# Kernel optimization log

Measured on AMD Instinct MI355X. Metric: run time of the kernel, lower is better.

The kernel has to match this reference:

```python
import jax, jax.numpy as jnp
import numpy as np

B, S, H, E, K, DFF = 4, 2048, 1024, 8, 2, 4096


def setup_inputs() -> dict:
    key = jax.random.key(0)
    k0, k1, k2, k3 = jax.random.split(key, 4)
    sc = 0.02
    return {
        "x": jax.random.normal(k0, (B, S, H), jnp.float32),
        "gate_W": jax.random.normal(k1, (H, E), jnp.float32) * sc,
        "gate_b": jnp.zeros((E,), jnp.float32),
        "W1": jax.random.normal(k2, (H, DFF), jnp.float32) * sc,
        "b1": jnp.zeros((DFF,), jnp.float32),
        "W2": jax.random.normal(k3, (DFF, H), jnp.float32) * sc,
        "b2": jnp.zeros((H,), jnp.float32),
    }


def reference(x, gate_W, gate_b, W1, b1, W2, b2):
    b, s, h = x.shape
    x_flat = x.reshape(-1, h)                      # [T, H]
    gate_scores = x_flat @ gate_W + gate_b         # [T, E]
    top_k_scores, top_k_idx = jax.lax.top_k(gate_scores, K)   # [T, K]
    top_k_w = jax.nn.softmax(top_k_scores, axis=-1)           # [T, K]

    # All experts share the same weights (ModuleList reuses one module), so
    # sum_i w_i * expert_i(x) == expert(x) * sum_i w_i. top_k indices are
    # unique per token, so the per-token combine weight is sum of top-k weights.
    hdd = jax.nn.gelu(x_flat @ W1 + b1, approximate=False)    # [T, DFF]
    y = hdd @ W2 + b2                                         # [T, H]
    tok_w = top_k_w.sum(axis=-1)                              # [T] (== 1.0)
    output = (y * tok_w[:, None]).reshape(b, s, h)

    expert_load = gate_scores.mean(axis=0)                    # [E]
    aux_loss = (expert_load ** 2).sum()
    exp_counts = jnp.zeros((E,), jnp.int32).at[top_k_idx.ravel()].add(1)
    return output, aux_loss, exp_counts
```

## Files before the change

### kernel.cpp

```cpp
#include <hip/hip_runtime.h>
#include <hip/hip_bf16.h>
#include <math.h>

#define Tn   8192
#define Hn   1024
#define En   8
#define DFFn 4096

typedef __attribute__((ext_vector_type(8))) short bf16x8;
typedef __attribute__((ext_vector_type(8))) unsigned short u16x8;
typedef __attribute__((ext_vector_type(4))) float f32x4;

static __device__ inline unsigned short f2bf(float f) {
    __hip_bfloat16 h = __float2bfloat16(f);
    return __builtin_bit_cast(unsigned short, h);
}

__global__ __launch_bounds__(256) void prep(
    const float* __restrict__ W1, unsigned short* __restrict__ W1t,
    const float* __restrict__ W2, unsigned short* __restrict__ W2t,
    const float* __restrict__ x, const float* __restrict__ gW,
    const float* __restrict__ gb, unsigned short* __restrict__ xbf,
    float* __restrict__ tokw, float* __restrict__ load_sum,
    int* __restrict__ counts)
{
    __shared__ float smem[8 * 1024 + En];
    __shared__ int   s_cnt[En];
    const int tid = threadIdx.x;
    const int id  = blockIdx.x;

    if (id < 512) {
        const float* src; unsigned short* dst; int SR, SC, tb;
        if (id < 256) { src = W1; dst = W1t; SR = Hn;   SC = DFFn; tb = id; }
        else          { src = W2; dst = W2t; SR = DFFn; SC = Hn;   tb = id - 256; }
        const int tcs = SC >> 7;
        const int tr  = tb / tcs, tc = tb - tr * tcs;
        const int r0  = tr << 7, c0 = tc << 7;
        unsigned short* tile = (unsigned short*)smem;

        #pragma unroll
        for (int i = 0; i < 16; ++i) {
            int idx = tid + i * 256;
            int r = idx >> 5, c4 = (idx & 31) << 2;
            float4 v = *(const float4*)(src + (size_t)(r0 + r) * SC + c0 + c4);
            int cs = c4 ^ (((r >> 3) & 7) << 2);
            ushort4 pk;
            pk.x = f2bf(v.x); pk.y = f2bf(v.y);
            pk.z = f2bf(v.z); pk.w = f2bf(v.w);
            *(ushort4*)(tile + r * 128 + cs) = pk;
        }
        __syncthreads();
        #pragma unroll
        for (int i = 0; i < 8; ++i) {
            int idx = tid + i * 256;
            int n = idx >> 4, kg = idx & 15, k0 = kg << 3;
            int s = (kg & 7) << 2;
            u16x8 o;
            #pragma unroll
            for (int j = 0; j < 8; ++j)
                o[j] = tile[(k0 + j) * 128 + (n ^ s)];
            *(u16x8*)(dst + (size_t)(c0 + n) * SR + r0 + k0) = o;
        }
        return;
    }

    const int gid = id - 512;
    float* gwt    = smem;
    float* s_load = smem + 8 * 1024;
    if (tid < En) { s_load[tid] = 0.f; s_cnt[tid] = 0; }
    #pragma unroll
    for (int i = 0; i < 32; ++i) {
        int f = tid + i * 256;
        gwt[(f & 7) * 1024 + (f >> 3)] = gW[f];
    }
    __syncthreads();

    const int lane = tid & 63;
    const int wv   = tid >> 6;

    for (int tok = gid * 4 + wv; tok < Tn; tok += 4096) {
        const float4* xr = (const float4*)(x + (size_t)tok * Hn);
        float acc[8] = {0.f,0.f,0.f,0.f,0.f,0.f,0.f,0.f};
        #pragma unroll
        for (int j = 0; j < Hn / 256; ++j) {
            int h4 = j * 64 + lane;
            float4 xv = xr[h4];
            ushort4 pk;
            pk.x = f2bf(xv.x); pk.y = f2bf(xv.y);
            pk.z = f2bf(xv.z); pk.w = f2bf(xv.w);
            ((ushort4*)xbf)[(size_t)tok * (Hn / 4) + h4] = pk;
            #pragma unroll
            for (int e = 0; e < 8; ++e) {
                const float4 w = *(const float4*)(gwt + e * 1024 + h4 * 4);
                acc[e] += xv.x * w.x + xv.y * w.y + xv.z * w.z + xv.w * w.w;
            }
        }
        #pragma unroll
        for (int e = 0; e < 8; ++e) {
            float v = acc[e];
            #pragma unroll
            for (int off = 32; off > 0; off >>= 1) v += __shfl_xor(v, off, 64);
            acc[e] = v + gb[e];
        }
        if (lane == 0) {
            #pragma unroll
            for (int e = 0; e < 8; ++e) atomicAdd(&s_load[e], acc[e]);
            int i1 = 0; float v1 = acc[0];
            #pragma unroll
            for (int e = 1; e < 8; ++e) if (acc[e] > v1) { v1 = acc[e]; i1 = e; }
            int i2 = -1; float v2 = -3.0e38f;
            #pragma unroll
            for (int e = 0; e < 8; ++e) if (e != i1 && acc[e] > v2) { v2 = acc[e]; i2 = e; }
            atomicAdd(&s_cnt[i1], 1);
            atomicAdd(&s_cnt[i2], 1);
            float e2 = __expf(v2 - v1);
            float t  = 1.0f + e2;
            tokw[tok] = 1.0f / t + e2 / t;
        }
    }
    __syncthreads();
    if (tid < En) {
        atomicAdd(&load_sum[tid], s_load[tid]);
        atomicAdd(&counts[tid],   s_cnt[tid]);
    }
}

static __device__ inline bf16x8 ldsfrag(const char* base, int row, int chunk) {
    return *(const bf16x8*)(base + row * 128 + (((chunk) ^ (row & 7)) << 4));
}

template<int BN, int WM, int WN, int EPI>
__global__ __launch_bounds__(512, 2) void gemm8(
    const __hip_bfloat16* __restrict__ A,
    const __hip_bfloat16* __restrict__ Bt,
    const float* __restrict__ bias,
    const float* __restrict__ tokw,
    void* __restrict__ C, int N, int K, int nx,
    const float* __restrict__ load_sum, const int* __restrict__ counts,
    float* __restrict__ out_tail, int nblk)
{
    constexpr int BM = 256;
    constexpr int MR = (BM / WM) / 16;
    constexpr int NR = (BN / WN) / 16;
    constexpr int AU = BM / 64;
    constexpr int BU = BN / 64;
    constexpr int ABYTES = BM * 64 * 2;
    constexpr int BBYTES = BN * 64 * 2;
    constexpr int TILEB  = ABYTES + BBYTES;

    extern __shared__ char lds[];

    const int tid = threadIdx.x;
    const int id  = blockIdx.x;

    if (EPI == 0 && id >= nblk) {
        if (tid == 0) {
            float aux = 0.f;
            #pragma unroll
            for (int e = 0; e < En; ++e) {
                float m = load_sum[e] * (1.0f / (float)Tn);
                aux += m * m;
            }
            out_tail[0] = aux;
            #pragma unroll
            for (int e = 0; e < En; ++e) out_tail[1 + e] = (float)counts[e];
        }
        return;
    }

    int wg = id;
    { int xcd = wg & 7, idx = wg >> 3; wg = xcd * (nblk >> 3) + idx; }
    const int by = wg / nx, bx = wg % nx;
    const int m0 = by * BM, n0 = bx * BN;

    const int lane = tid & 63;
    const int wid  = tid >> 6;
    const int wn   = wid % WN;
    const int wm   = wid / WN;
    const int wrow = wm * (BM / WM);
    const int wcol = wn * (BN / WN);
    const int fr   = lane & 15;
    const int fq   = lane >> 4;

    const int sr = tid >> 3;
    const int sc = (tid & 7) ^ (sr & 7);
    unsigned aOff[AU], bOff[BU];
    #pragma unroll
    for (int u = 0; u < AU; ++u)
        aOff[u] = (unsigned)((m0 + u * 64 + sr) * K + sc * 8);
    #pragma unroll
    for (int u = 0; u < BU; ++u)
        bOff[u] = (unsigned)((n0 + u * 64 + sr) * K + sc * 8);

#define STA(b, u, kt) __builtin_amdgcn_global_load_lds( \
    (const __attribute__((address_space(1))) void*)(A + aOff[u] + (unsigned)(kt) * 64u), \
    (__attribute__((address_space(3))) void*)(lds + (b) * TILEB + (u) * 8192 + tid * 16), 16, 0, 0)
#define STB(b, u, kt) __builtin_amdgcn_global_load_lds( \
    (const __attribute__((address_space(1))) void*)(Bt + bOff[u] + (unsigned)(kt) * 64u), \
    (__attribute__((address_space(3))) void*)(lds + (b) * TILEB + ABYTES + (u) * 8192 + tid * 16), 16, 0, 0)

    bf16x8 af[MR / 2][2];
    bf16x8 bfr[4][2];
    f32x4  acc[MR][NR];
    const f32x4 zero = {0.f, 0.f, 0.f, 0.f};
    #pragma unroll
    for (int i = 0; i < MR; ++i)
        #pragma unroll
        for (int j = 0; j < NR; ++j) acc[i][j] = zero;

#define RD_A1(b, half, m_) do { _Pragma("unroll") \
    for (int ks_ = 0; ks_ < 2; ++ks_) \
        af[m_][ks_] = ldsfrag(lds + (b) * TILEB, \
            wrow + ((half) * (MR / 2) + (m_)) * 16 + fr, ks_ * 4 + fq); } while (0)
#define RD_B1(b, nn) do { _Pragma("unroll") \
    for (int ks_ = 0; ks_ < 2; ++ks_) \
        bfr[nn][ks_] = ldsfrag(lds + (b) * TILEB + ABYTES, \
            wcol + (nn) * 16 + fr, ks_ * 4 + fq); } while (0)

#define MFMA_M(hm, hn, m_) do { _Pragma("unroll") \
    for (int n_ = 0; n_ < 2; ++n_) { _Pragma("unroll") \
        for (int ks_ = 0; ks_ < 2; ++ks_) \
            acc[(hm) * (MR / 2) + (m_)][(hn) * 2 + n_] = \
                __builtin_amdgcn_mfma_f32_16x16x32_bf16( \
                    af[m_][ks_], bfr[(hn) * 2 + n_][ks_], \
                    acc[(hm) * (MR / 2) + (m_)][(hn) * 2 + n_], 0, 0, 0); } } while (0)
#define MFMA_N(hm, nn) do { _Pragma("unroll") \
    for (int m_ = 0; m_ < MR / 2; ++m_) { _Pragma("unroll") \
        for (int ks_ = 0; ks_ < 2; ++ks_) \
            acc[(hm) * (MR / 2) + m_][nn] = \
                __builtin_amdgcn_mfma_f32_16x16x32_bf16( \
                    af[m_][ks_], bfr[nn][ks_], \
                    acc[(hm) * (MR / 2) + m_][nn], 0, 0, 0); } } while (0)

#define MFMA1_N(hm, nn) do { _Pragma("unroll") \
    for (int m_ = 0; m_ < MR / 2; ++m_) { _Pragma("unroll") \
        for (int ks_ = 0; ks_ < 2; ++ks_) \
            acc[(hm) * (MR / 2) + m_][nn] = \
                __builtin_amdgcn_mfma_f32_16x16x32_bf16( \
                    bfr[nn][ks_], af[m_][ks_], \
                    acc[(hm) * (MR / 2) + m_][nn], 0, 0, 0); } } while (0)
#define MFMA1_M(hm, m_) do { _Pragma("unroll") \
    for (int n_ = 0; n_ < NR; ++n_) { _Pragma("unroll") \
        for (int ks_ = 0; ks_ < 2; ++ks_) \
            acc[(hm) * (MR / 2) + (m_)][n_] = \
                __builtin_amdgcn_mfma_f32_16x16x32_bf16( \
                    bfr[n_][ks_], af[m_][ks_], \
                    acc[(hm) * (MR / 2) + (m_)][n_], 0, 0, 0); } } while (0)

#define SBAR do { \
    __builtin_amdgcn_sched_barrier(0); \
    __builtin_amdgcn_s_barrier(); \
    __builtin_amdgcn_sched_barrier(0); } while (0)
#define WAITL(n) do { \
    asm volatile("s_waitcnt lgkmcnt(" #n ")" ::: "memory"); \
    __builtin_amdgcn_sched_barrier(0); } while (0)
#define PRIO1 __builtin_amdgcn_s_setprio(1)
#define PRIO0 __builtin_amdgcn_s_setprio(0)
#define DRAIN6 do { asm volatile("s_waitcnt vmcnt(6)" ::: "memory"); \
    __builtin_amdgcn_sched_barrier(0); } while (0)
#define DRAIN2 do { asm volatile("s_waitcnt vmcnt(2)" ::: "memory"); \
    __builtin_amdgcn_sched_barrier(0); } while (0)

    const int KT = K >> 6;

    if constexpr (WM == 2) {
        STA(0,0,0); STA(0,1,0); STA(0,2,0); STA(0,3,0);
        STB(0,0,0); STB(0,1,0); STB(0,2,0); STB(0,3,0);
        STA(1,0,1); STA(1,2,1);
        STB(1,0,1); STB(1,1,1); STB(1,2,1); STB(1,3,1);
        DRAIN6;
        __builtin_amdgcn_s_barrier();
        __builtin_amdgcn_sched_barrier(0);

        for (int i = 0; i < (KT >> 1); ++i) {
            const int t1 = 2 * i + 1;
            const int c2 = (2 * i + 2 < KT) ? 2 * i + 2 : KT - 1;
            const int c3 = (2 * i + 3 < KT) ? 2 * i + 3 : KT - 1;

            RD_B1(0,0); RD_B1(0,1);
            RD_A1(0,0,0); RD_A1(0,0,1); RD_A1(0,0,2); RD_A1(0,0,3);
            STA(1,1,t1); STA(1,3,t1);
            SBAR; PRIO1;
            WAITL(6); MFMA_M(0,0,0);
            WAITL(4); MFMA_M(0,0,1);
            WAITL(2); MFMA_M(0,0,2);
            WAITL(0); MFMA_M(0,0,3);
            PRIO0; SBAR;
            RD_B1(0,2); RD_B1(0,3);
            STA(0,0,c2); STA(0,2,c2);
            SBAR; PRIO1;
            WAITL(2); MFMA_N(0,2);
            WAITL(0); MFMA_N(0,3);
            PRIO0; SBAR;
            RD_A1(0,1,0); RD_A1(0,1,1); RD_A1(0,1,2); RD_A1(0,1,3);
            STB(0,0,c2); STB(0,1,c2);
            SBAR; PRIO1;
            WAITL(6); MFMA_M(1,0,0);
            WAITL(4); MFMA_M(1,0,1);
            WAITL(2); MFMA_M(1,0,2);
            WAITL(0); MFMA_M(1,0,3);
            PRIO0; SBAR;
            STB(0,2,c2); STB(0,3,c2);
            SBAR; PRIO1;
            MFMA_M(1,1,0); MFMA_M(1,1,1); MFMA_M(1,1,2); MFMA_M(1,1,3);
            PRIO0; DRAIN6; SBAR;
            RD_B1(1,0); RD_B1(1,1);
            RD_A1(1,0,0); RD_A1(1,0,1); RD_A1(1,0,2); RD_A1(1,0,3);
            STA(0,1,c2); STA(0,3,c2);
            SBAR; PRIO1;
            WAITL(6); MFMA_M(0,0,0);
            WAITL(4); MFMA_M(0,0,1);
            WAITL(2); MFMA_M(0,0,2);
            WAITL(0); MFMA_M(0,0,3);
            PRIO0; SBAR;
            RD_B1(1,2); RD_B1(1,3);
            STA(1,0,c3); STA(1,2,c3);
            SBAR; PRIO1;
            WAITL(2); MFMA_N(0,2);
            WAITL(0); MFMA_N(0,3);
            PRIO0; SBAR;
            RD_A1(1,1,0); RD_A1(1,1,1); RD_A1(1,1,2); RD_A1(1,1,3);
            STB(1,0,c3); STB(1,1,c3);
            SBAR; PRIO1;
            WAITL(6); MFMA_M(1,0,0);
            WAITL(4); MFMA_M(1,0,1);
            WAITL(2); MFMA_M(1,0,2);
            WAITL(0); MFMA_M(1,0,3);
            PRIO0; SBAR;
            STB(1,2,c3); STB(1,3,c3);
            SBAR; PRIO1;
            MFMA_M(1,1,0); MFMA_M(1,1,1); MFMA_M(1,1,2); MFMA_M(1,1,3);
            PRIO0; DRAIN6; SBAR;
        }

        float bias4[NR];
        #pragma unroll
        for (int ni = 0; ni < NR; ++ni)
            bias4[ni] = bias[n0 + wcol + ni * 16 + fr];
        #pragma unroll
        for (int mi = 0; mi < MR; ++mi) {
            #pragma unroll
            for (int ni = 0; ni < NR; ++ni) {
                const int col = n0 + wcol + ni * 16 + fr;
                const int rb  = m0 + wrow + mi * 16 + fq * 4;
                #pragma unroll
                for (int i2 = 0; i2 < 4; ++i2) {
                    float u  = acc[mi][ni][i2] + bias4[ni];
                    float uu = u * u;
                    float z  = u * __fmaf_rn(uu, -0.07135607f, -1.59576912f);
                    float e  = __expf(z);
                    float g  = u * __builtin_amdgcn_rcpf(1.0f + e);
                    ((__hip_bfloat16*)C)[(size_t)(rb + i2) * N + col] =
                        __float2bfloat16(g);
                }
            }
        }
    } else {
        STA(0,0,0); STA(0,1,0); STA(0,2,0); STA(0,3,0);
        STB(0,0,0); STB(0,1,0);
        STB(1,0,1); STB(1,1,1);
        DRAIN2;
        __builtin_amdgcn_s_barrier();
        __builtin_amdgcn_sched_barrier(0);

        for (int i = 0; i < (KT >> 1); ++i) {
            const int t1 = 2 * i + 1;
            const int c2 = (2 * i + 2 < KT) ? 2 * i + 2 : KT - 1;
            const int c3 = (2 * i + 3 < KT) ? 2 * i + 3 : KT - 1;

            RD_A1(0,0,0); RD_A1(0,0,1);
            RD_B1(0,0); RD_B1(0,1); RD_B1(0,2); RD_B1(0,3);
            STA(1,0,t1); STA(1,1,t1); STA(1,2,t1); STA(1,3,t1);
            SBAR; PRIO1;
            WAITL(6); MFMA1_N(0,0);
            WAITL(4); MFMA1_N(0,1);
            WAITL(2); MFMA1_N(0,2);
            WAITL(0); MFMA1_N(0,3);
            PRIO0; SBAR;
            RD_A1(0,1,0); RD_A1(0,1,1);
            STB(0,0,c2); STB(0,1,c2);
            SBAR; PRIO1;
            WAITL(2); MFMA1_M(1,0);
            WAITL(0); MFMA1_M(1,1);
            PRIO0; DRAIN2; SBAR;
            RD_A1(1,0,0); RD_A1(1,0,1);
            RD_B1(1,0); RD_B1(1,1); RD_B1(1,2); RD_B1(1,3);
            STA(0,0,c2); STA(0,1,c2); STA(0,2,c2); STA(0,3,c2);
            SBAR; PRIO1;
            WAITL(6); MFMA1_N(0,0);
            WAITL(4); MFMA1_N(0,1);
            WAITL(2); MFMA1_N(0,2);
            WAITL(0); MFMA1_N(0,3);
            PRIO0; SBAR;
            RD_A1(1,1,0); RD_A1(1,1,1);
            STB(1,0,c3); STB(1,1,c3);
            SBAR; PRIO1;
            WAITL(2); MFMA1_M(1,0);
            WAITL(0); MFMA1_M(1,1);
            PRIO0; DRAIN2; SBAR;
        }

        const int mrow0 = m0 + wrow + fr;
        const int ncol0 = n0 + wcol + fq * 4;
        float4 b4[NR];
        #pragma unroll
        for (int ni = 0; ni < NR; ++ni)
            b4[ni] = *(const float4*)(bias + ncol0 + ni * 16);

        #pragma unroll
        for (int mi = 0; mi < MR; ++mi) {
            const int row = mrow0 + mi * 16;
            const float tw = tokw[row];
            #pragma unroll
            for (int ni = 0; ni < NR; ++ni) {
                f32x4 v = acc[mi][ni];
                float4 o;
                o.x = (v[0] + b4[ni].x) * tw;
                o.y = (v[1] + b4[ni].y) * tw;
                o.z = (v[2] + b4[ni].z) * tw;
                o.w = (v[3] + b4[ni].w) * tw;
                *(float4*)((float*)C + (size_t)row * N + ncol0 + ni * 16) = o;
            }
        }
    }

#undef STA
#undef STB
#undef RD_A1
#undef RD_B1
#undef MFMA_M
#undef MFMA_N
#undef MFMA1_N
#undef MFMA1_M
#undef SBAR
#undef WAITL
#undef PRIO1
#undef PRIO0
#undef DRAIN6
#undef DRAIN2
}

extern "C" void kernel_launch(void* const* d_in, const int* in_sizes, int n_in,
                              void* d_out, int out_size, void* d_ws, size_t ws_size,
                              hipStream_t stream)
{
    const float* x  = (const float*)d_in[0];
    const float* gW = (const float*)d_in[1];
    const float* gb = (const float*)d_in[2];
    const float* W1 = (const float*)d_in[3];
    const float* b1 = (const float*)d_in[4];
    const float* W2 = (const float*)d_in[5];
    const float* b2 = (const float*)d_in[6];
    float* out = (float*)d_out;

    char* ws = (char*)d_ws;
    __hip_bfloat16* xbf = (__hip_bfloat16*)ws;  ws += (size_t)Tn * Hn * 2;
    __hip_bfloat16* W1t = (__hip_bfloat16*)ws;  ws += (size_t)Hn * DFFn * 2;
    __hip_bfloat16* W2t = (__hip_bfloat16*)ws;  ws += (size_t)Hn * DFFn * 2;
    __hip_bfloat16* hdd = (__hip_bfloat16*)ws;  ws += (size_t)Tn * DFFn * 2;
    float* tokw     = (float*)ws;               ws += (size_t)Tn * 4;
    float* load_sum = (float*)ws;               ws += En * 4;
    int*   counts   = (int*)ws;                 ws += En * 4;

    static bool attr_done = false;
    if (!attr_done) {
        (void)hipFuncSetAttribute(
            reinterpret_cast<const void*>(&gemm8<256, 2, 4, 0>),
            hipFuncAttributeMaxDynamicSharedMemorySize, 131072);
        (void)hipFuncSetAttribute(
            reinterpret_cast<const void*>(&gemm8<128, 4, 2, 1>),
            hipFuncAttributeMaxDynamicSharedMemorySize, 98304);
        attr_done = true;
    }

    hipMemsetAsync(load_sum, 0, En * 4 * 2, stream);

    prep<<<1536, 256, 0, stream>>>(W1, (unsigned short*)W1t,
                                   W2, (unsigned short*)W2t,
                                   x, gW, gb, (unsigned short*)xbf,
                                   tokw, load_sum, counts);

    gemm8<256, 2, 4, 0><<<513, 512, 131072, stream>>>(
        xbf, W1t, b1, nullptr, hdd, DFFn, Hn, 16,
        load_sum, counts, out + (size_t)Tn * Hn, 512);

    gemm8<128, 4, 2, 1><<<256, 512, 98304, stream>>>(
        hdd, W2t, b2, tokw, out, Hn, DFFn, 8,
        nullptr, nullptr, nullptr, 256);
}
```

Baseline: 267.7 us.

## Restructure first GEMM MFMA schedule and replace gating atomics with per-block partials

The first GEMM's inner loop now loads whole fragment groups and waits once at a combined barrier plus lgkmcnt(0), in place of staggered per-fragment waits. Each MFMA quadrant is wrapped in priority raises. The gating stage now runs with fewer blocks, each handling more tokens. It writes per-block load and count partials instead of global atomics, which removes the memset, and the tail block of GEMM1 reduces those partials. The gating weights are also loaded as float4. The coarser waits give up some overlap between LDS reads and MFMAs in exchange for fewer scheduling points.

```diff
diff --git a/kernel.cpp b/kernel.cpp
--- a/kernel.cpp
+++ b/kernel.cpp
@@ -21,8 +21,8 @@
     const float* __restrict__ W2, unsigned short* __restrict__ W2t,
     const float* __restrict__ x, const float* __restrict__ gW,
     const float* __restrict__ gb, unsigned short* __restrict__ xbf,
-    float* __restrict__ tokw, float* __restrict__ load_sum,
-    int* __restrict__ counts)
+    float* __restrict__ tokw, float* __restrict__ pb_load,
+    int* __restrict__ pb_cnt)
 {
     __shared__ float smem[8 * 1024 + En];
     __shared__ int   s_cnt[En];
@@ -69,16 +69,21 @@
     float* s_load = smem + 8 * 1024;
     if (tid < En) { s_load[tid] = 0.f; s_cnt[tid] = 0; }
     #pragma unroll
-    for (int i = 0; i < 32; ++i) {
-        int f = tid + i * 256;
-        gwt[(f & 7) * 1024 + (f >> 3)] = gW[f];
+    for (int i = 0; i < 8; ++i) {
+        int f4 = tid + i * 256;
+        float4 v = ((const float4*)gW)[f4];
+        int f = f4 << 2;
+        gwt[((f + 0) & 7) * 1024 + ((f + 0) >> 3)] = v.x;
+        gwt[((f + 1) & 7) * 1024 + ((f + 1) >> 3)] = v.y;
+        gwt[((f + 2) & 7) * 1024 + ((f + 2) >> 3)] = v.z;
+        gwt[((f + 3) & 7) * 1024 + ((f + 3) >> 3)] = v.w;
     }
     __syncthreads();
 
     const int lane = tid & 63;
     const int wv   = tid >> 6;
 
-    for (int tok = gid * 4 + wv; tok < Tn; tok += 4096) {
+    for (int tok = gid * 4 + wv; tok < Tn; tok += 1024) {
         const float4* xr = (const float4*)(x + (size_t)tok * Hn);
         float acc[8] = {0.f,0.f,0.f,0.f,0.f,0.f,0.f,0.f};
         #pragma unroll
@@ -120,8 +125,8 @@
     }
     __syncthreads();
     if (tid < En) {
-        atomicAdd(&load_sum[tid], s_load[tid]);
-        atomicAdd(&counts[tid],   s_cnt[tid]);
+        pb_load[gid * En + tid] = s_load[tid];
+        pb_cnt [gid * En + tid] = s_cnt[tid];
     }
 }
 
@@ -136,7 +141,7 @@
     const float* __restrict__ bias,
     const float* __restrict__ tokw,
     void* __restrict__ C, int N, int K, int nx,
-    const float* __restrict__ load_sum, const int* __restrict__ counts,
+    const float* __restrict__ pb_load, const int* __restrict__ pb_cnt,
     float* __restrict__ out_tail, int nblk)
 {
     constexpr int BM = 256;
@@ -154,16 +159,29 @@
     const int id  = blockIdx.x;
 
     if (EPI == 0 && id >= nblk) {
+        float* sl = (float*)lds;
+        int*   sc = (int*)(lds + 64);
+        if (tid < En) { sl[tid] = 0.f; sc[tid] = 0; }
+        __syncthreads();
+        const int e = tid & 7;
+        float p = 0.f; int c = 0;
+        for (int g = tid >> 3; g < 256; g += 64) {
+            p += pb_load[g * En + e];
+            c += pb_cnt [g * En + e];
+        }
+        atomicAdd(&sl[e], p);
+        atomicAdd(&sc[e], c);
+        __syncthreads();
         if (tid == 0) {
             float aux = 0.f;
             #pragma unroll
-            for (int e = 0; e < En; ++e) {
-                float m = load_sum[e] * (1.0f / (float)Tn);
+            for (int e2 = 0; e2 < En; ++e2) {
+                float m = sl[e2] * (1.0f / (float)Tn);
                 aux += m * m;
             }
             out_tail[0] = aux;
             #pragma unroll
-            for (int e = 0; e < En; ++e) out_tail[1 + e] = (float)counts[e];
+            for (int e2 = 0; e2 < En; ++e2) out_tail[1 + e2] = (float)sc[e2];
         }
         return;
     }
@@ -208,29 +226,29 @@
         #pragma unroll
         for (int j = 0; j < NR; ++j) acc[i][j] = zero;
 
-#define RD_A1(b, half, m_) do { _Pragma("unroll") \
-    for (int ks_ = 0; ks_ < 2; ++ks_) \
-        af[m_][ks_] = ldsfrag(lds + (b) * TILEB, \
-            wrow + ((half) * (MR / 2) + (m_)) * 16 + fr, ks_ * 4 + fq); } while (0)
-#define RD_B1(b, nn) do { _Pragma("unroll") \
-    for (int ks_ = 0; ks_ < 2; ++ks_) \
-        bfr[nn][ks_] = ldsfrag(lds + (b) * TILEB + ABYTES, \
-            wcol + (nn) * 16 + fr, ks_ * 4 + fq); } while (0)
-
-#define MFMA_M(hm, hn, m_) do { _Pragma("unroll") \
+#define RDA(b, half) do { _Pragma("unroll") \
+    for (int m_ = 0; m_ < MR / 2; ++m_) { _Pragma("unroll") \
+        for (int ks_ = 0; ks_ < 2; ++ks_) \
+            af[m_][ks_] = ldsfrag(lds + (b) * TILEB, \
+                wrow + ((half) * (MR / 2) + m_) * 16 + fr, ks_ * 4 + fq); } } while (0)
+
+#define RDB(b, half) do { _Pragma("unroll") \
     for (int n_ = 0; n_ < 2; ++n_) { _Pragma("unroll") \
         for (int ks_ = 0; ks_ < 2; ++ks_) \
-            acc[(hm) * (MR / 2) + (m_)][(hn) * 2 + n_] = \
-                __builtin_amdgcn_mfma_f32_16x16x32_bf16( \
-                    af[m_][ks_], bfr[(hn) * 2 + n_][ks_], \
-                    acc[(hm) * (MR / 2) + (m_)][(hn) * 2 + n_], 0, 0, 0); } } while (0)
-#define MFMA_N(hm, nn) do { _Pragma("unroll") \
+            bfr[(half) * 2 + n_][ks_] = ldsfrag(lds + (b) * TILEB + ABYTES, \
+                wcol + ((half) * 2 + n_) * 16 + fr, ks_ * 4 + fq); } } while (0)
+
+#define MFMAQ(hm, hn) do { \
+    __builtin_amdgcn_s_setprio(1); \
+    _Pragma("unroll") \
     for (int m_ = 0; m_ < MR / 2; ++m_) { _Pragma("unroll") \
-        for (int ks_ = 0; ks_ < 2; ++ks_) \
-            acc[(hm) * (MR / 2) + m_][nn] = \
-                __builtin_amdgcn_mfma_f32_16x16x32_bf16( \
-                    af[m_][ks_], bfr[nn][ks_], \
-                    acc[(hm) * (MR / 2) + m_][nn], 0, 0, 0); } } while (0)
+        for (int n_ = 0; n_ < 2; ++n_) { _Pragma("unroll") \
+            for (int ks_ = 0; ks_ < 2; ++ks_) \
+                acc[(hm) * (MR / 2) + m_][(hn) * 2 + n_] = \
+                    __builtin_amdgcn_mfma_f32_16x16x32_bf16( \
+                        af[m_][ks_], bfr[(hn) * 2 + n_][ks_], \
+                        acc[(hm) * (MR / 2) + m_][(hn) * 2 + n_], 0, 0, 0); } } \
+    __builtin_amdgcn_s_setprio(0); } while (0)
 
 #define MFMA1_N(hm, nn) do { _Pragma("unroll") \
     for (int m_ = 0; m_ < MR / 2; ++m_) { _Pragma("unroll") \
@@ -247,19 +265,36 @@
                     bfr[n_][ks_], af[m_][ks_], \
                     acc[(hm) * (MR / 2) + (m_)][n_], 0, 0, 0); } } while (0)
 
-#define SBAR do { \
+#define RD_A1(b, half, m_) do { _Pragma("unroll") \
+    for (int ks_ = 0; ks_ < 2; ++ks_) \
+        af[m_][ks_] = ldsfrag(lds + (b) * TILEB, \
+            wrow + ((half) * (MR / 2) + (m_)) * 16 + fr, ks_ * 4 + fq); } while (0)
+#define RD_B1(b, nn) do { _Pragma("unroll") \
+    for (int ks_ = 0; ks_ < 2; ++ks_) \
+        bfr[nn][ks_] = ldsfrag(lds + (b) * TILEB + ABYTES, \
+            wcol + (nn) * 16 + fr, ks_ * 4 + fq); } while (0)
+
+#define MIDSYNC do { \
+    __builtin_amdgcn_sched_barrier(0); \
+    __builtin_amdgcn_s_barrier(); \
+    asm volatile("s_waitcnt lgkmcnt(0)" ::: "memory"); \
+    __builtin_amdgcn_sched_barrier(0); } while (0)
+
+#define SBARR do { \
     __builtin_amdgcn_sched_barrier(0); \
     __builtin_amdgcn_s_barrier(); \
     __builtin_amdgcn_sched_barrier(0); } while (0)
+
 #define WAITL(n) do { \
     asm volatile("s_waitcnt lgkmcnt(" #n ")" ::: "memory"); \
     __builtin_amdgcn_sched_barrier(0); } while (0)
-#define PRIO1 __builtin_amdgcn_s_setprio(1)
-#define PRIO0 __builtin_amdgcn_s_setprio(0)
+
 #define DRAIN6 do { asm volatile("s_waitcnt vmcnt(6)" ::: "memory"); \
     __builtin_amdgcn_sched_barrier(0); } while (0)
 #define DRAIN2 do { asm volatile("s_waitcnt vmcnt(2)" ::: "memory"); \
     __builtin_amdgcn_sched_barrier(0); } while (0)
+#define PRIO1 __builtin_amdgcn_s_setprio(1)
+#define PRIO0 __builtin_amdgcn_s_setprio(0)
 
     const int KT = K >> 6;
 
@@ -277,60 +312,28 @@
             const int c2 = (2 * i + 2 < KT) ? 2 * i + 2 : KT - 1;
             const int c3 = (2 * i + 3 < KT) ? 2 * i + 3 : KT - 1;
 
-            RD_B1(0,0); RD_B1(0,1);
-            RD_A1(0,0,0); RD_A1(0,0,1); RD_A1(0,0,2); RD_A1(0,0,3);
+            RDA(0, 0); RDB(0, 0);
             STA(1,1,t1); STA(1,3,t1);
-            SBAR; PRIO1;
-            WAITL(6); MFMA_M(0,0,0);
-            WAITL(4); MFMA_M(0,0,1);
-            WAITL(2); MFMA_M(0,0,2);
-            WAITL(0); MFMA_M(0,0,3);
-            PRIO0; SBAR;
-            RD_B1(0,2); RD_B1(0,3);
+            MIDSYNC; MFMAQ(0, 0); SBARR;
+            RDB(0, 1);
             STA(0,0,c2); STA(0,2,c2);
-            SBAR; PRIO1;
-            WAITL(2); MFMA_N(0,2);
-            WAITL(0); MFMA_N(0,3);
-            PRIO0; SBAR;
-            RD_A1(0,1,0); RD_A1(0,1,1); RD_A1(0,1,2); RD_A1(0,1,3);
+            MIDSYNC; MFMAQ(0, 1); SBARR;
+            RDA(0, 1);
             STB(0,0,c2); STB(0,1,c2);
-            SBAR; PRIO1;
-            WAITL(6); MFMA_M(1,0,0);
-            WAITL(4); MFMA_M(1,0,1);
-            WAITL(2); MFMA_M(1,0,2);
-            WAITL(0); MFMA_M(1,0,3);
-            PRIO0; SBAR;
+            MIDSYNC; MFMAQ(1, 0); SBARR;
             STB(0,2,c2); STB(0,3,c2);
-            SBAR; PRIO1;
-            MFMA_M(1,1,0); MFMA_M(1,1,1); MFMA_M(1,1,2); MFMA_M(1,1,3);
-            PRIO0; DRAIN6; SBAR;
-            RD_B1(1,0); RD_B1(1,1);
-            RD_A1(1,0,0); RD_A1(1,0,1); RD_A1(1,0,2); RD_A1(1,0,3);
+            MIDSYNC; MFMAQ(1, 1); DRAIN6; SBARR;
+            RDA(1, 0); RDB(1, 0);
             STA(0,1,c2); STA(0,3,c2);
-            SBAR; PRIO1;
-            WAITL(6); MFMA_M(0,0,0);
-            WAITL(4); MFMA_M(0,0,1);
-            WAITL(2); MFMA_M(0,0,2);
-            WAITL(0); MFMA_M(0,0,3);
-            PRIO0; SBAR;
-            RD_B1(1,2); RD_B1(1,3);
+            MIDSYNC; MFMAQ(0, 0); SBARR;
+            RDB(1, 1);
             STA(1,0,c3); STA(1,2,c3);
-            SBAR; PRIO1;
-            WAITL(2); MFMA_N(0,2);
-            WAITL(0); MFMA_N(0,3);
-            PRIO0; SBAR;
-            RD_A1(1,1,0); RD_A1(1,1,1); RD_A1(1,1,2); RD_A1(1,1,3);
+            MIDSYNC; MFMAQ(0, 1); SBARR;
+            RDA(1, 1);
             STB(1,0,c3); STB(1,1,c3);
-            SBAR; PRIO1;
-            WAITL(6); MFMA_M(1,0,0);
-            WAITL(4); MFMA_M(1,0,1);
-            WAITL(2); MFMA_M(1,0,2);
-            WAITL(0); MFMA_M(1,0,3);
-            PRIO0; SBAR;
+            MIDSYNC; MFMAQ(1, 0); SBARR;
             STB(1,2,c3); STB(1,3,c3);
-            SBAR; PRIO1;
-            MFMA_M(1,1,0); MFMA_M(1,1,1); MFMA_M(1,1,2); MFMA_M(1,1,3);
-            PRIO0; DRAIN6; SBAR;
+            MIDSYNC; MFMAQ(1, 1); DRAIN6; SBARR;
         }
 
         float bias4[NR];
@@ -371,33 +374,33 @@
             RD_A1(0,0,0); RD_A1(0,0,1);
             RD_B1(0,0); RD_B1(0,1); RD_B1(0,2); RD_B1(0,3);
             STA(1,0,t1); STA(1,1,t1); STA(1,2,t1); STA(1,3,t1);
-            SBAR; PRIO1;
+            SBARR; PRIO1;
             WAITL(6); MFMA1_N(0,0);
             WAITL(4); MFMA1_N(0,1);
             WAITL(2); MFMA1_N(0,2);
             WAITL(0); MFMA1_N(0,3);
-            PRIO0; SBAR;
+            PRIO0; SBARR;
             RD_A1(0,1,0); RD_A1(0,1,1);
             STB(0,0,c2); STB(0,1,c2);
-            SBAR; PRIO1;
+            SBARR; PRIO1;
             WAITL(2); MFMA1_M(1,0);
             WAITL(0); MFMA1_M(1,1);
-            PRIO0; DRAIN2; SBAR;
+            PRIO0; DRAIN2; SBARR;
             RD_A1(1,0,0); RD_A1(1,0,1);
             RD_B1(1,0); RD_B1(1,1); RD_B1(1,2); RD_B1(1,3);
             STA(0,0,c2); STA(0,1,c2); STA(0,2,c2); STA(0,3,c2);
-            SBAR; PRIO1;
+            SBARR; PRIO1;
             WAITL(6); MFMA1_N(0,0);
             WAITL(4); MFMA1_N(0,1);
             WAITL(2); MFMA1_N(0,2);
             WAITL(0); MFMA1_N(0,3);
-            PRIO0; SBAR;
+            PRIO0; SBARR;
             RD_A1(1,1,0); RD_A1(1,1,1);
             STB(1,0,c3); STB(1,1,c3);
-            SBAR; PRIO1;
+            SBARR; PRIO1;
             WAITL(2); MFMA1_M(1,0);
             WAITL(0); MFMA1_M(1,1);
-            PRIO0; DRAIN2; SBAR;
+            PRIO0; DRAIN2; SBARR;
         }
 
         const int mrow0 = m0 + wrow + fr;
@@ -426,18 +429,20 @@
 
 #undef STA
 #undef STB
+#undef RDA
+#undef RDB
 #undef RD_A1
 #undef RD_B1
-#undef MFMA_M
-#undef MFMA_N
+#undef MFMAQ
 #undef MFMA1_N
 #undef MFMA1_M
-#undef SBAR
+#undef MIDSYNC
+#undef SBARR
 #undef WAITL
+#undef DRAIN6
+#undef DRAIN2
 #undef PRIO1
 #undef PRIO0
-#undef DRAIN6
-#undef DRAIN2
 }
 
 extern "C" void kernel_launch(void* const* d_in, const int* in_sizes, int n_in,
@@ -459,8 +464,8 @@
     __hip_bfloat16* W2t = (__hip_bfloat16*)ws;  ws += (size_t)Hn * DFFn * 2;
     __hip_bfloat16* hdd = (__hip_bfloat16*)ws;  ws += (size_t)Tn * DFFn * 2;
     float* tokw     = (float*)ws;               ws += (size_t)Tn * 4;
-    float* load_sum = (float*)ws;               ws += En * 4;
-    int*   counts   = (int*)ws;                 ws += En * 4;
+    float* pb_load  = (float*)ws;               ws += 256 * En * 4;
+    int*   pb_cnt   = (int*)ws;                 ws += 256 * En * 4;
 
     static bool attr_done = false;
     if (!attr_done) {
@@ -473,16 +478,14 @@
         attr_done = true;
     }
 
-    hipMemsetAsync(load_sum, 0, En * 4 * 2, stream);
-
-    prep<<<1536, 256, 0, stream>>>(W1, (unsigned short*)W1t,
-                                   W2, (unsigned short*)W2t,
-                                   x, gW, gb, (unsigned short*)xbf,
-                                   tokw, load_sum, counts);
+    prep<<<768, 256, 0, stream>>>(W1, (unsigned short*)W1t,
+                                  W2, (unsigned short*)W2t,
+                                  x, gW, gb, (unsigned short*)xbf,
+                                  tokw, pb_load, pb_cnt);
 
     gemm8<256, 2, 4, 0><<<513, 512, 131072, stream>>>(
         xbf, W1t, b1, nullptr, hdd, DFFn, Hn, 16,
-        load_sum, counts, out + (size_t)Tn * Hn, 512);
+        pb_load, pb_cnt, out + (size_t)Tn * Hn, 512);
 
     gemm8<128, 4, 2, 1><<<256, 512, 98304, stream>>>(
         hdd, W2t, b2, tokw, out, Hn, DFFn, 8,
```

New measurement: 262.9 us. About the same (-1.8%).
